# Kernel tuning notes

Measured on AMD Instinct MI355X. Metric: run time of the kernel, lower is better.

## Reference

```python
import jax, jax.numpy as jnp
import numpy as np

NUM_LAYERS = 4
EMBED = 1024
HEADS = 16
QKV = 1024
MLP = 4096
EPS_LN = 1e-6


def _layernorm(x, scale, bias):
    m = jnp.mean(x, axis=-1, keepdims=True)
    v = jnp.mean(jnp.square(x - m), axis=-1, keepdims=True)
    return (x - m) * jax.lax.rsqrt(v + EPS_LN) * scale + bias


def setup_inputs() -> dict:
    key = jax.random.key(0)
    ks = jax.random.split(key, 12)
    B, L = 4, 1024
    s = 0.02
    inp = {
        "queries": jax.random.normal(ks[0], (B, L, EMBED), dtype=jnp.float32),
        "Wq": jax.random.normal(ks[1], (NUM_LAYERS, EMBED, QKV), dtype=jnp.float32) * s,
        "bq": jnp.zeros((NUM_LAYERS, QKV), dtype=jnp.float32),
        "Wk": jax.random.normal(ks[2], (NUM_LAYERS, EMBED, QKV), dtype=jnp.float32) * s,
        "bk": jnp.zeros((NUM_LAYERS, QKV), dtype=jnp.float32),
        "Wv": jax.random.normal(ks[3], (NUM_LAYERS, EMBED, QKV), dtype=jnp.float32) * s,
        "bv": jnp.zeros((NUM_LAYERS, QKV), dtype=jnp.float32),
        "Wo": jax.random.normal(ks[4], (NUM_LAYERS, QKV, EMBED), dtype=jnp.float32) * s,
        "bo": jnp.zeros((NUM_LAYERS, EMBED), dtype=jnp.float32),
        "ln1_s": jnp.ones((NUM_LAYERS, EMBED), dtype=jnp.float32),
        "ln1_b": jnp.zeros((NUM_LAYERS, EMBED), dtype=jnp.float32),
        "ln2_s": jnp.ones((NUM_LAYERS, EMBED), dtype=jnp.float32),
        "ln2_b": jnp.zeros((NUM_LAYERS, EMBED), dtype=jnp.float32),
        "W1": jax.random.normal(ks[5], (NUM_LAYERS, EMBED, MLP), dtype=jnp.float32) * s,
        "b1": jnp.zeros((NUM_LAYERS, MLP), dtype=jnp.float32),
        "W2": jax.random.normal(ks[6], (NUM_LAYERS, MLP, EMBED), dtype=jnp.float32) * s,
        "b2": jnp.zeros((NUM_LAYERS, EMBED), dtype=jnp.float32),
    }
    return inp


def _block(x, Wq, bq, Wk, bk, Wv, bv, Wo, bo, ln1_s, ln1_b, ln2_s, ln2_b, W1, b1, W2, b2):
    # post-norm block (pre_norm=False)
    B, L, _ = x.shape
    head_dim = EMBED // HEADS
    q = (x @ Wq + bq).reshape(B, L, HEADS, head_dim)
    k = (x @ Wk + bk).reshape(B, L, HEADS, head_dim)
    v = (x @ Wv + bv).reshape(B, L, HEADS, head_dim)
    q = q / (head_dim ** 0.5)
    attn = jnp.einsum("bqhd,bkhd->bhqk", q, k)
    attn = jax.nn.softmax(attn, axis=-1)
    upd = jnp.einsum("bhqk,bkhd->bqhd", attn, v)  # [B,L,H,hd]
    a = upd.reshape(B, L, QKV) @ Wo + bo
    h = _layernorm(a + x, ln1_s, ln1_b)
    z = jax.nn.relu(h @ W1 + b1) @ W2 + b2
    return _layernorm(z + h, ln2_s, ln2_b)


def reference(queries, Wq, bq, Wk, bk, Wv, bv, Wo, bo, ln1_s, ln1_b, ln2_s, ln2_b, W1, b1, W2, b2):
    x = queries
    for l in range(NUM_LAYERS):
        x = _block(x, Wq[l], bq[l], Wk[l], bk[l], Wv[l], bv[l], Wo[l], bo[l],
                   ln1_s[l], ln1_b[l], ln2_s[l], ln2_b[l], W1[l], b1[l], W2[l], b2[l])
    return x
```

## Files before the change

### kernel.cpp

```cpp
#include <hip/hip_runtime.h>
#include <stdint.h>

typedef __bf16 bf16;
typedef __bf16 bf16x8 __attribute__((ext_vector_type(8)));
typedef float floatx4 __attribute__((ext_vector_type(4)));

#define LOG2E 1.44269504088896340736f

__device__ __forceinline__ void gl2lds16(const bf16* g, bf16* l) {
    __builtin_amdgcn_global_load_lds((__attribute__((address_space(1))) void*)g,
                                     (__attribute__((address_space(3))) void*)l,
                                     16, 0, 0);
}

template<int COLS>
__device__ __forceinline__ int swz(int ch, int r) {
    if constexpr (COLS == 32) return ch ^ ((r >> 1) & 3);
    else                      return ch ^ (r & 7);
}

template<int ROWS, int COLS>
__device__ __forceinline__ void stage_tile_sw(bf16* lds, const bf16* g, int srcStride, int wave, int lane) {
    constexpr int NINST = (ROWS * COLS * 2) / 1024;
    constexpr int ROWB  = COLS * 2;
    #pragma unroll
    for (int u = 0; u < NINST / 4; ++u) {
        int t  = wave + u * 4;
        int ob = t * 1024 + lane * 16;
        int r  = ob / ROWB;
        int ch = (ob % ROWB) >> 4;
        int sc = swz<COLS>(ch, r);
        gl2lds16(g + r * srcStride + sc * 8, lds + t * 512);
    }
}

template<int RELU, int OUTF, int OUTB>
__device__ __forceinline__ void gemm_core(const bf16* __restrict__ A, const bf16* __restrict__ Bt,
                                          const float* __restrict__ bias, float scale,
                                          float* __restrict__ outf, bf16* __restrict__ outb,
                                          int M, int N, int K, int m0, int n0) {
    __shared__ bf16 As[128 * 32];
    __shared__ bf16 Bs[128 * 32];
    const int tid = threadIdx.x, wave = tid >> 6, lane = tid & 63;
    const int wr = wave >> 1, wc = wave & 1;
    const int quad = lane >> 4, lq = lane & 15;
    const int swa = quad ^ ((lq >> 1) & 3);

    floatx4 acc[4][4] = {};
    const bf16* Ap = A + (size_t)m0 * K;
    const bf16* Bp = Bt + (size_t)n0 * K;

    for (int k0 = 0; k0 < K; k0 += 32) {
        stage_tile_sw<128, 32>(As, Ap + k0, K, wave, lane);
        stage_tile_sw<128, 32>(Bs, Bp + k0, K, wave, lane);
        __syncthreads();
        bf16x8 af[4], bfr[4];
        #pragma unroll
        for (int i = 0; i < 4; i++)
            af[i] = *(const bf16x8*)&As[(wr * 64 + i * 16 + lq) * 32 + swa * 8];
        #pragma unroll
        for (int j = 0; j < 4; j++)
            bfr[j] = *(const bf16x8*)&Bs[(wc * 64 + j * 16 + lq) * 32 + swa * 8];
        #pragma unroll
        for (int i = 0; i < 4; i++)
            #pragma unroll
            for (int j = 0; j < 4; j++)
                acc[i][j] = __builtin_amdgcn_mfma_f32_16x16x32_bf16(af[i], bfr[j], acc[i][j], 0, 0, 0);
        __syncthreads();
    }
    #pragma unroll
    for (int j = 0; j < 4; j++) {
        const int gc = n0 + wc * 64 + j * 16 + lq;
        const float bv = bias[gc];
        #pragma unroll
        for (int i = 0; i < 4; i++) {
            #pragma unroll
            for (int r = 0; r < 4; r++) {
                const int gr = m0 + wr * 64 + i * 16 + quad * 4 + r;
                float v = (acc[i][j][r] + bv) * scale;
                if (RELU) v = fmaxf(v, 0.f);
                if (OUTF) outf[(size_t)gr * N + gc] = v;
                if (OUTB) outb[(size_t)gr * N + gc] = (bf16)v;
            }
        }
    }
}

__global__ __launch_bounds__(256) void gemm_bf16relu(const bf16* A, const bf16* Bt, const float* bias,
                                                     bf16* out) {
    const int bid = blockIdx.x;
    const int xcd = bid & 7, j = bid >> 3;
    const int mt = xcd * 4 + (j >> 5);
    const int nt = j & 31;
    gemm_core<1, 0, 1>(A, Bt, bias, 1.f, nullptr, out, 4096, 4096, 1024, mt * 128, nt * 128);
}

__global__ __launch_bounds__(256) void gemm_qkv(const bf16* A, const bf16* Wt,
                                                const float* bq, const float* bk, const float* bv,
                                                bf16* out) {
    const int bid = blockIdx.x;
    const int xcd = bid & 7, j = bid >> 3;
    const int mloc = j / 24, r = j % 24;
    const int z = r >> 3, nt = r & 7;
    const int mt = xcd * 4 + mloc;
    const bf16* Bt = Wt + (size_t)z * 1024 * 1024;
    const float* bias = (z == 0) ? bq : (z == 1) ? bk : bv;
    bf16* o = out + (size_t)z * 4096 * 1024;
    const float scale = (z == 0) ? 0.125f * LOG2E : 1.f;
    gemm_core<0, 0, 1>(A, Bt, bias, scale, nullptr, o, 4096, 1024, 1024, mt * 128, nt * 128);
}

__global__ __launch_bounds__(256) void gemm_n1024(const bf16* __restrict__ A, const bf16* __restrict__ Bt,
                                                  const float* __restrict__ bias, float* __restrict__ out,
                                                  int K) {
    __shared__ bf16 As[128 * 64];
    __shared__ bf16 Bs[64 * 64];
    const int bid = blockIdx.x;
    const int xcd = bid & 7, j = bid >> 3;
    const int sk = j >> 6, j2 = j & 63;
    const int mt = xcd * 4 + (j2 >> 4);
    const int nt = j2 & 15;
    const int m0 = mt * 128, n0 = nt * 64;
    const int Kh = K >> 1;
    const int tid = threadIdx.x, wave = tid >> 6, lane = tid & 63;
    const int wr = wave >> 1, wc = wave & 1;
    const int quad = lane >> 4, lq = lane & 15;

    floatx4 acc[4][2] = {};
    const bf16* Ap = A + (size_t)m0 * K + (size_t)sk * Kh;
    const bf16* Bp = Bt + (size_t)n0 * K + (size_t)sk * Kh;

    for (int k0 = 0; k0 < Kh; k0 += 64) {
        stage_tile_sw<128, 64>(As, Ap + k0, K, wave, lane);
        stage_tile_sw<64, 64>(Bs, Bp + k0, K, wave, lane);
        __syncthreads();
        #pragma unroll
        for (int kk = 0; kk < 2; kk++) {
            const int chs = ((kk * 4 + quad) ^ (lq & 7)) * 8;
            bf16x8 af[4], bfr[2];
            #pragma unroll
            for (int i = 0; i < 4; i++)
                af[i] = *(const bf16x8*)&As[(wr * 64 + i * 16 + lq) * 64 + chs];
            #pragma unroll
            for (int jj = 0; jj < 2; jj++)
                bfr[jj] = *(const bf16x8*)&Bs[(wc * 32 + jj * 16 + lq) * 64 + chs];
            #pragma unroll
            for (int i = 0; i < 4; i++)
                #pragma unroll
                for (int jj = 0; jj < 2; jj++)
                    acc[i][jj] = __builtin_amdgcn_mfma_f32_16x16x32_bf16(af[i], bfr[jj], acc[i][jj], 0, 0, 0);
        }
        __syncthreads();
    }
    float* op = out + (size_t)sk * 4194304;
    #pragma unroll
    for (int jj = 0; jj < 2; jj++) {
        const int gc = n0 + wc * 32 + jj * 16 + lq;
        const float bv = sk ? 0.f : bias[gc];
        #pragma unroll
        for (int i = 0; i < 4; i++)
            #pragma unroll
            for (int r = 0; r < 4; r++) {
                const int gr = m0 + wr * 64 + i * 16 + quad * 4 + r;
                op[(size_t)gr * 1024 + gc] = acc[i][jj][r] + bv;
            }
    }
}

__device__ __forceinline__ void ttile(const float* __restrict__ src, bf16* __restrict__ dst,
                                      int K, int N, int n0, int k0) {
    __shared__ float t[32][33];
    const int tx = threadIdx.x & 31, ty = threadIdx.x >> 5;
    #pragma unroll
    for (int i = 0; i < 4; i++)
        t[ty + i * 8][tx] = src[(size_t)(k0 + ty + i * 8) * N + n0 + tx];
    __syncthreads();
    #pragma unroll
    for (int i = 0; i < 4; i++)
        dst[(size_t)(n0 + ty + i * 8) * K + k0 + tx] = (bf16)t[tx][ty + i * 8];
}

__global__ __launch_bounds__(256) void transpose_all(const float* Wq, const float* Wk, const float* Wv,
                                                     const float* Wo, const float* W1, const float* W2,
                                                     bf16* qkvT, bf16* oT, bf16* w1T, bf16* w2T) {
    const int bx = blockIdx.x;
    if (bx < 4096) {
        const int z = bx >> 10, tile = bx & 1023;
        const float* s = (z == 0) ? Wq : (z == 1) ? Wk : (z == 2) ? Wv : Wo;
        bf16* d = (z == 3) ? oT : qkvT + (size_t)z * 1048576;
        ttile(s, d, 1024, 1024, (tile & 31) * 32, (tile >> 5) * 32);
    } else if (bx < 8192) {
        const int tile = bx - 4096;
        ttile(W1, w1T, 1024, 4096, (tile & 127) * 32, (tile >> 7) * 32);
    } else {
        const int tile = bx - 8192;
        ttile(W2, w2T, 4096, 1024, (tile & 31) * 32, (tile >> 5) * 32);
    }
}

__global__ __launch_bounds__(256) void transpose_v(const bf16* v, bf16* vT) {
    __shared__ bf16 t[32][33];
    const int l0 = blockIdx.x * 32, d0 = blockIdx.y * 32, bh = blockIdx.z;
    const int b = bh >> 4, h = bh & 15;
    const int tx = threadIdx.x & 31, ty = threadIdx.x >> 5;
    #pragma unroll
    for (int i = 0; i < 4; i++)
        t[ty + i * 8][tx] = v[(size_t)(b * 1024 + l0 + ty + i * 8) * 1024 + h * 64 + d0 + tx];
    __syncthreads();
    #pragma unroll
    for (int i = 0; i < 4; i++)
        vT[((size_t)bh * 64 + d0 + ty + i * 8) * 1024 + l0 + tx] = t[tx][ty + i * 8];
}

__global__ __launch_bounds__(256) void cvt_f32_bf16(const float* src, bf16* dst) {
    const int i = (blockIdx.x * 256 + threadIdx.x) * 4;
    const float4 v = *(const float4*)(src + i);
    bf16 t4[4] = {(bf16)v.x, (bf16)v.y, (bf16)v.z, (bf16)v.w};
    *(uint64_t*)(dst + i) = *(const uint64_t*)t4;
}

__global__ __launch_bounds__(256) void ln_kernel(const float* __restrict__ a, const float* __restrict__ a2,
                                                 const float* __restrict__ res,
                                                 const float* __restrict__ gamma, const float* __restrict__ beta,
                                                 float* __restrict__ outf, bf16* __restrict__ outb) {
    const int row = blockIdx.x, tid = threadIdx.x;
    const size_t base = (size_t)row * 1024 + tid * 4;
    const float4 av  = *(const float4*)(a + base);
    const float4 a2v = *(const float4*)(a2 + base);
    const float4 rv  = *(const float4*)(res + base);
    float x0 = av.x + a2v.x + rv.x, x1 = av.y + a2v.y + rv.y;
    float x2 = av.z + a2v.z + rv.z, x3 = av.w + a2v.w + rv.w;
    float s  = x0 + x1 + x2 + x3;
    float sq = x0 * x0 + x1 * x1 + x2 * x2 + x3 * x3;
    #pragma unroll
    for (int off = 32; off; off >>= 1) {
        s  += __shfl_xor(s,  off, 64);
        sq += __shfl_xor(sq, off, 64);
    }
    __shared__ float red[8];
    const int wave = tid >> 6, lane = tid & 63;
    if (lane == 0) { red[wave] = s; red[wave + 4] = sq; }
    __syncthreads();
    const float S  = red[0] + red[1] + red[2] + red[3];
    const float SQ = red[4] + red[5] + red[6] + red[7];
    const float mean = S * (1.f / 1024.f);
    const float var  = SQ * (1.f / 1024.f) - mean * mean;
    const float rstd = rsqrtf(var + 1e-6f);
    const int c = tid * 4;
    const float4 g  = *(const float4*)(gamma + c);
    const float4 be = *(const float4*)(beta + c);
    float y0 = (x0 - mean) * rstd * g.x + be.x;
    float y1 = (x1 - mean) * rstd * g.y + be.y;
    float y2 = (x2 - mean) * rstd * g.z + be.z;
    float y3 = (x3 - mean) * rstd * g.w + be.w;
    float4 yo; yo.x = y0; yo.y = y1; yo.z = y2; yo.w = y3;
    *(float4*)(outf + base) = yo;
    bf16 t4[4] = {(bf16)y0, (bf16)y1, (bf16)y2, (bf16)y3};
    *(uint64_t*)(outb + base) = *(const uint64_t*)t4;
}

__global__ __launch_bounds__(256, 2) void attn_kernel(const bf16* __restrict__ Q, const bf16* __restrict__ Kg,
                                                      const bf16* __restrict__ Vt, bf16* __restrict__ O) {
    __shared__ bf16 Ks[128 * 64];
    __shared__ bf16 Vs[64 * 128];
    __shared__ bf16 Ps[128 * 128];
    const int bh = blockIdx.x, qt = blockIdx.y;
    const int b = bh >> 4, h = bh & 15;
    const int tid = threadIdx.x, wave = tid >> 6, lane = tid & 63;
    const int quad = lane >> 4, lq = lane & 15;

    const bf16* qg = Q + ((size_t)b * 1024 + qt * 128) * 1024 + h * 64;
    const bf16* kg = Kg + (size_t)b * 1024 * 1024 + h * 64;
    const bf16* vg = Vt + (size_t)bh * 64 * 1024;

    stage_tile_sw<128, 64>(Ps, qg, 1024, wave, lane);
    __syncthreads();
    bf16x8 aq[2][2];
    #pragma unroll
    for (int i = 0; i < 2; i++)
        #pragma unroll
        for (int kk = 0; kk < 2; kk++) {
            const int row = wave * 32 + i * 16 + lq;
            const int chs = (kk * 4 + quad) ^ (lq & 7);
            aq[i][kk] = *(const bf16x8*)&Ps[row * 64 + chs * 8];
        }

    floatx4 oacc[2][4] = {};
    float lsum[2][4] = {};

    for (int kt = 0; kt < 1024; kt += 128) {
        stage_tile_sw<128, 64>(Ks, kg + (size_t)kt * 1024, 1024, wave, lane);
        stage_tile_sw<64, 128>(Vs, vg + kt, 1024, wave, lane);
        __syncthreads();

        floatx4 sacc[2][8] = {};
        #pragma unroll
        for (int kk = 0; kk < 2; kk++)
            #pragma unroll
            for (int j = 0; j < 8; j++) {
                const int chs = (kk * 4 + quad) ^ (lq & 7);
                bf16x8 bk = *(const bf16x8*)&Ks[(j * 16 + lq) * 64 + chs * 8];
                sacc[0][j] = __builtin_amdgcn_mfma_f32_16x16x32_bf16(aq[0][kk], bk, sacc[0][j], 0, 0, 0);
                sacc[1][j] = __builtin_amdgcn_mfma_f32_16x16x32_bf16(aq[1][kk], bk, sacc[1][j], 0, 0, 0);
            }

        #pragma unroll
        for (int i = 0; i < 2; i++)
            #pragma unroll
            for (int r = 0; r < 4; r++) {
                const int row = wave * 32 + i * 16 + quad * 4 + r;
                const int rb = row & 7;
                float ls = 0.f;
                #pragma unroll
                for (int j = 0; j < 8; j++) {
                    const float pv = exp2f(sacc[i][j][r]);
                    ls += pv;
                    const int col = j * 16 + lq;
                    Ps[row * 128 + ((col >> 3) ^ rb) * 8 + (col & 7)] = (bf16)pv;
                }
                lsum[i][r] += ls;
            }

        #pragma unroll
        for (int kk = 0; kk < 4; kk++) {
            bf16x8 ap[2];
            #pragma unroll
            for (int i = 0; i < 2; i++) {
                const int row = wave * 32 + i * 16 + lq;
                const int chs = (kk * 4 + quad) ^ (lq & 7);
                ap[i] = *(const bf16x8*)&Ps[row * 128 + chs * 8];
            }
            #pragma unroll
            for (int dj = 0; dj < 4; dj++) {
                const int chs = (kk * 4 + quad) ^ (lq & 7);
                bf16x8 bv = *(const bf16x8*)&Vs[(dj * 16 + lq) * 128 + chs * 8];
                oacc[0][dj] = __builtin_amdgcn_mfma_f32_16x16x32_bf16(ap[0], bv, oacc[0][dj], 0, 0, 0);
                oacc[1][dj] = __builtin_amdgcn_mfma_f32_16x16x32_bf16(ap[1], bv, oacc[1][dj], 0, 0, 0);
            }
        }
        __syncthreads();
    }

    #pragma unroll
    for (int i = 0; i < 2; i++)
        #pragma unroll
        for (int r = 0; r < 4; r++) {
            float l = lsum[i][r];
            l += __shfl_xor(l, 1, 64); l += __shfl_xor(l, 2, 64);
            l += __shfl_xor(l, 4, 64); l += __shfl_xor(l, 8, 64);
            lsum[i][r] = 1.f / l;
        }
    #pragma unroll
    for (int i = 0; i < 2; i++)
        #pragma unroll
        for (int dj = 0; dj < 4; dj++)
            #pragma unroll
            for (int r = 0; r < 4; r++) {
                const int row = qt * 128 + wave * 32 + i * 16 + quad * 4 + r;
                O[((size_t)b * 1024 + row) * 1024 + h * 64 + dj * 16 + lq] = (bf16)(oacc[i][dj][r] * lsum[i][r]);
            }
}

extern "C" void kernel_launch(void* const* d_in, const int* in_sizes, int n_in,
                              void* d_out, int out_size, void* d_ws, size_t ws_size,
                              hipStream_t stream) {
    const float* queries = (const float*)d_in[0];
    const float* Wq = (const float*)d_in[1];  const float* bq = (const float*)d_in[2];
    const float* Wk = (const float*)d_in[3];  const float* bk = (const float*)d_in[4];
    const float* Wv = (const float*)d_in[5];  const float* bv = (const float*)d_in[6];
    const float* Wo = (const float*)d_in[7];  const float* bo = (const float*)d_in[8];
    const float* ln1_s = (const float*)d_in[9];   const float* ln1_b = (const float*)d_in[10];
    const float* ln2_s = (const float*)d_in[11];  const float* ln2_b = (const float*)d_in[12];
    const float* W1 = (const float*)d_in[13]; const float* b1 = (const float*)d_in[14];
    const float* W2 = (const float*)d_in[15]; const float* b2 = (const float*)d_in[16];

    char* p = (char*)d_ws;
    size_t off = 0;
    auto take = [&](size_t bytes) { void* r = p + off; off += bytes; return r; };
    bf16*  WqkvT = (bf16*)take(6291456);
    bf16*  WoT   = (bf16*)take(2097152);
    bf16*  W1T   = (bf16*)take(8388608);
    bf16*  W2T   = (bf16*)take(8388608);
    bf16*  x_bf  = (bf16*)take(8388608);
    float* xf    = (float*)take(16777216);
    bf16*  qkvb  = (bf16*)take(25165824);
    bf16*  vTb   = (bf16*)take(8388608);
    bf16*  updb  = (bf16*)take(8388608);
    float* az    = (float*)take(33554432);
    float* hf    = (float*)take(16777216);
    bf16*  hbf   = (bf16*)take(8388608);
    bf16*  tmlp  = (bf16*)take(33554432);

    cvt_f32_bf16<<<4096, 256, 0, stream>>>(queries, x_bf);

    for (int l = 0; l < 4; ++l) {
        const size_t w1k = (size_t)l * 1024 * 1024;
        const size_t w4m = (size_t)l * 4096 * 1024;
        transpose_all<<<12288, 256, 0, stream>>>(Wq + w1k, Wk + w1k, Wv + w1k, Wo + w1k,
                                                 W1 + w4m, W2 + w4m, WqkvT, WoT, W1T, W2T);

        gemm_qkv<<<768, 256, 0, stream>>>(x_bf, WqkvT,
                                          bq + l * 1024, bk + l * 1024, bv + l * 1024, qkvb);
        transpose_v<<<dim3(32, 2, 64), 256, 0, stream>>>(qkvb + 2 * 4194304, vTb);
        attn_kernel<<<dim3(64, 8), 256, 0, stream>>>(qkvb, qkvb + 4194304, vTb, updb);
        gemm_n1024<<<1024, 256, 0, stream>>>(updb, WoT, bo + l * 1024, az, 1024);
        ln_kernel<<<4096, 256, 0, stream>>>(az, az + 4194304, (l == 0) ? queries : xf,
                                            ln1_s + l * 1024, ln1_b + l * 1024, hf, hbf);
        gemm_bf16relu<<<1024, 256, 0, stream>>>(hbf, W1T, b1 + l * 4096, tmlp);
        gemm_n1024<<<1024, 256, 0, stream>>>(tmlp, W2T, b2 + l * 1024, az, 4096);
        ln_kernel<<<4096, 256, 0, stream>>>(az, az + 4194304, hf, ln2_s + l * 1024, ln2_b + l * 1024,
                                            (l == 3) ? (float*)d_out : xf, x_bf);
    }
}
```

Before: 1.153 ms.

## Permute key order in V transpose so attention stores P rows as vectors

```diff
diff --git a/kernel.cpp b/kernel.cpp
--- a/kernel.cpp
+++ b/kernel.cpp
@@ -199,17 +199,30 @@
 }
 
 __global__ __launch_bounds__(256) void transpose_v(const bf16* v, bf16* vT) {
-    __shared__ bf16 t[32][33];
-    const int l0 = blockIdx.x * 32, d0 = blockIdx.y * 32, bh = blockIdx.z;
+    __shared__ float t[128][34];
+    const int l0 = blockIdx.x * 128, d0 = blockIdx.y * 32, bh = blockIdx.z;
     const int b = bh >> 4, h = bh & 15;
-    const int tx = threadIdx.x & 31, ty = threadIdx.x >> 5;
-    #pragma unroll
-    for (int i = 0; i < 4; i++)
-        t[ty + i * 8][tx] = v[(size_t)(b * 1024 + l0 + ty + i * 8) * 1024 + h * 64 + d0 + tx];
+    const int tid = threadIdx.x;
+    const int dp = (tid & 15) * 2, lr = tid >> 4;
+    #pragma unroll
+    for (int i = 0; i < 8; i++) {
+        const int lrow = lr + i * 16;
+        bf16 two[2];
+        *(uint32_t*)two = *(const uint32_t*)&v[(size_t)(b * 1024 + l0 + lrow) * 1024 + h * 64 + d0 + dp];
+        t[lrow][dp]     = (float)two[0];
+        t[lrow][dp + 1] = (float)two[1];
+    }
     __syncthreads();
     #pragma unroll
-    for (int i = 0; i < 4; i++)
-        vT[((size_t)bh * 64 + d0 + ty + i * 8) * 1024 + l0 + tx] = t[tx][ty + i * 8];
+    for (int u2 = 0; u2 < 2; u2++) {
+        const int c = tid + u2 * 256;
+        const int d = c >> 4, lp = c & 15;
+        bf16 pb[8];
+        #pragma unroll
+        for (int j = 0; j < 8; j++)
+            pb[j] = (bf16)t[j * 16 + lp][d];
+        *(bf16x8*)&vT[((size_t)bh * 64 + d0 + d) * 1024 + l0 + lp * 8] = *(bf16x8*)pb;
+    }
 }
 
 __global__ __launch_bounds__(256) void cvt_f32_bf16(const float* src, bf16* dst) {
@@ -309,16 +322,16 @@
             #pragma unroll
             for (int r = 0; r < 4; r++) {
                 const int row = wave * 32 + i * 16 + quad * 4 + r;
-                const int rb = row & 7;
                 float ls = 0.f;
+                bf16 pb[8];
                 #pragma unroll
                 for (int j = 0; j < 8; j++) {
                     const float pv = exp2f(sacc[i][j][r]);
                     ls += pv;
-                    const int col = j * 16 + lq;
-                    Ps[row * 128 + ((col >> 3) ^ rb) * 8 + (col & 7)] = (bf16)pv;
+                    pb[j] = (bf16)pv;
                 }
                 lsum[i][r] += ls;
+                *(bf16x8*)&Ps[row * 128 + (lq ^ (row & 7)) * 8] = *(const bf16x8*)pb;
             }
 
         #pragma unroll
@@ -401,7 +414,7 @@
 
         gemm_qkv<<<768, 256, 0, stream>>>(x_bf, WqkvT,
                                           bq + l * 1024, bk + l * 1024, bv + l * 1024, qkvb);
-        transpose_v<<<dim3(32, 2, 64), 256, 0, stream>>>(qkvb + 2 * 4194304, vTb);
+        transpose_v<<<dim3(8, 2, 64), 256, 0, stream>>>(qkvb + 2 * 4194304, vTb);
         attn_kernel<<<dim3(64, 8), 256, 0, stream>>>(qkvb, qkvb + 4194304, vTb, updb);
         gemm_n1024<<<1024, 256, 0, stream>>>(updb, WoT, bo + l * 1024, az, 1024);
         ln_kernel<<<4096, 256, 0, stream>>>(az, az + 4194304, (l == 0) ? queries : xf,
```

New measurement: 1.089 ms. -5.5%, faster.
